# Kernel tuning notes

Measured on AMD Instinct MI355X. Metric: run time of the kernel, lower is better.

Reference implementation:

```python
import jax, jax.numpy as jnp
import numpy as np

N_NODES = 100000
N_EDGES = 1600000
IN_FEATS = 128
N_HIDDEN = 128
N_CLASSES = 47


def _glorot(key, shape):
    fan_in, fan_out = shape
    lim = jnp.sqrt(6.0 / (fan_in + fan_out))
    return jax.random.uniform(key, shape, jnp.float32, -lim, lim)


def setup_inputs() -> dict:
    key = jax.random.key(0)
    ks = jax.random.split(key, 12)
    x = jax.random.normal(ks[0], (N_NODES, IN_FEATS), jnp.float32)
    src = jax.random.randint(ks[1], (N_EDGES,), 0, N_NODES, jnp.int32)
    dst = jax.random.randint(ks[2], (N_EDGES,), 0, N_NODES, jnp.int32)
    dims = [(IN_FEATS, N_HIDDEN), (N_HIDDEN, N_HIDDEN), (N_HIDDEN, N_CLASSES)]
    params = {}
    for l, (di, do) in enumerate(dims):
        params[f"Ws{l}"] = _glorot(ks[3 + 3 * l], (di, do))
        params[f"Wn{l}"] = _glorot(ks[4 + 3 * l], (di, do))
        params[f"b{l}"] = jnp.zeros((do,), jnp.float32)
    return {"x": x, "src": src, "dst": dst, **params}


def _sage_layer(h, src, dst, Ws, Wn, b):
    # mean aggregation over incoming edges (irregular gather + segment-reduce)
    n = h.shape[0]
    msg = h[src]  # [E, F]
    agg = jax.ops.segment_sum(msg, dst, num_segments=n)
    deg = jax.ops.segment_sum(jnp.ones((src.shape[0],), h.dtype), dst, num_segments=n)
    agg = agg / jnp.maximum(deg, 1.0)[:, None]
    return h @ Ws + agg @ Wn + b


def reference(x, src, dst, Ws0, Wn0, b0, Ws1, Wn1, b1, Ws2, Wn2, b2):
    layers = [(Ws0, Wn0, b0), (Ws1, Wn1, b1), (Ws2, Wn2, b2)]
    h = x
    for l, (Ws, Wn, b) in enumerate(layers):
        h = _sage_layer(h, src, dst, Ws, Wn, b)
        if l != len(layers) - 1:
            h = jax.nn.relu(h)  # dropout is identity at inference
    return h
```

## Files before the change

kernel.cpp:

```cpp
#include <hip/hip_runtime.h>
#include <cstdint>
#include <cstddef>

static const int NN = 100000;
static const int NE = 1600000;
static const int F  = 128;
static const int BKT_SHIFT = 7;
static const int BNODES = 1 << BKT_SHIFT;
static const int NBKT = (NN + BNODES - 1) >> BKT_SHIFT;
static const int PKCAP = 4096;
static const int SRC_BITS = 17;
static const unsigned SRC_MASK = (1u << SRC_BITS) - 1u;

static const int GM = (NN + 127)/128;
static const int PREPW_B = 320;

typedef __attribute__((ext_vector_type(8))) short short8;
typedef __attribute__((ext_vector_type(4))) float float4v;
typedef __attribute__((ext_vector_type(2))) float f32x2;

static __device__ __forceinline__ unsigned f2bf(float f){
    unsigned u = __builtin_bit_cast(unsigned, f);
    return (u + 0x7FFFu + ((u >> 16) & 1u)) >> 16;
}
static __device__ __forceinline__ float bf_lo(unsigned u){
    return __builtin_bit_cast(float, u << 16);
}
static __device__ __forceinline__ float bf_hi(unsigned u){
    return __builtin_bit_cast(float, u & 0xFFFF0000u);
}


__global__ __launch_bounds__(256) void prep_fused_k(
        const int* __restrict__ src, const int* __restrict__ dst,
        int* __restrict__ bfill, unsigned* __restrict__ pk,
        const float* __restrict__ Ws0, const float* __restrict__ Wn0,
        const float* __restrict__ Ws1, const float* __restrict__ Wn1,
        const float* __restrict__ Ws2, const float* __restrict__ Wn2,
        unsigned short* __restrict__ Wt0, unsigned short* __restrict__ Wt1,
        unsigned short* __restrict__ Wt2){
    __shared__ int sh[2*NBKT];
    const int bid = blockIdx.x;
    const int t = threadIdx.x;
    if (bid < NBKT){
        int* hist  = sh;
        int* gbase = sh + NBKT;
        for (int i = t; i < NBKT; i += 256) hist[i] = 0;
        __syncthreads();
        const int e0 = bid * 2048;
        int s[8], d[8], b[8], r[8];
        #pragma unroll
        for (int j = 0; j < 8; ++j){
            int e = e0 + j*256 + t;
            if (e < NE){
                s[j] = src[e]; d[j] = dst[e];
                b[j] = d[j] >> BKT_SHIFT;
                r[j] = atomicAdd(&hist[b[j]], 1);
            }
        }
        __syncthreads();
        for (int i = t; i < NBKT; i += 256){
            int h = hist[i];
            int base = 0;
            if (h) base = atomicAdd(&bfill[i], h);
            gbase[i] = i*PKCAP + base;
        }
        __syncthreads();
        #pragma unroll
        for (int j = 0; j < 8; ++j){
            int e = e0 + j*256 + t;
            if (e < NE)
                pk[gbase[b[j]] + r[j]] =
                    (unsigned)s[j] | ((unsigned)(d[j] & (BNODES-1)) << SRC_BITS);
        }
    } else {
        int i = (bid - NBKT)*256 + t;
        const float* Ws; const float* Wn; unsigned short* Wt; int D; int idx;
        if (i < 32768){       Ws=Ws0; Wn=Wn0; Wt=Wt0; D=128; idx=i; }
        else if (i < 65536){  Ws=Ws1; Wn=Wn1; Wt=Wt1; D=128; idx=i-32768; }
        else {                Ws=Ws2; Wn=Wn2; Wt=Wt2; D=47;  idx=i-65536; }
        int n = idx >> 7, k = idx & 127;
        float v = 0.f;
        if (n < D)        v = Ws[k*D + n];
        else if (n < 2*D) v = Wn[k*D + (n - D)];
        Wt[n*128 + k] = (unsigned short)f2bf(v);
    }
}


template<int WN>
static __device__ __forceinline__ void gemm_core(char* ldsA,
        const unsigned short* __restrict__ Wt, const float* __restrict__ bias,
        unsigned short* __restrict__ Y, unsigned short* __restrict__ Z,
        int M, int D, int Dpad, int tile, int cbase){
    const int t = threadIdx.x;
    const int lane = t & 63;
    const int w = t >> 6;
    const int wm = w / WN, wn = w % WN;

    short8 bfrag[4][4];
    {
        int ncol = cbase + wn*64;
        #pragma unroll
        for (int n = 0; n < 4; ++n){
            int wrow = ncol + n*16 + (lane & 15);
            const unsigned short* bp = Wt + (size_t)wrow*128 + ((lane >> 4) * 8);
            #pragma unroll
            for (int kk = 0; kk < 4; ++kk)
                bfrag[n][kk] = *(const short8*)(bp + kk*32);
        }
    }

    float4v acc[4][4];
    #pragma unroll
    for (int m = 0; m < 4; ++m)
        #pragma unroll
        for (int n = 0; n < 4; ++n)
            acc[m][n] = (float4v){0.f,0.f,0.f,0.f};

    __syncthreads();

    #pragma unroll
    for (int m = 0; m < 4; ++m){
        int r = wm*64 + m*16 + (lane & 15);
        #pragma unroll
        for (int kk = 0; kk < 4; ++kk){
            int c = kk*4 + (lane >> 4);
            short8 a = *(const short8*)(ldsA + (size_t)r*256 + ((size_t)(c ^ (r & 7)) << 4));
            #pragma unroll
            for (int n = 0; n < 4; ++n)
                acc[m][n] = __builtin_amdgcn_mfma_f32_16x16x32_bf16(a, bfrag[n][kk], acc[m][n], 0, 0, 0);
        }
    }

    #pragma unroll
    for (int m = 0; m < 4; ++m){
        #pragma unroll
        for (int n = 0; n < 4; ++n){
            int c = cbase + wn*64 + n*16 + (lane & 15);
            #pragma unroll
            for (int j = 0; j < 4; ++j){
                int r = tile + wm*64 + m*16 + (lane >> 4)*4 + j;
                if (r < M){
                    float v = acc[m][n][j];
                    if (c < D){
                        v += bias[c];
                        Y[(size_t)r*Dpad + c] = (unsigned short)f2bf(v);
                    } else if (c < 2*D){
                        Z[(size_t)r*Dpad + (c - D)] = (unsigned short)f2bf(v);
                    }
                }
            }
        }
    }
}

template<int WAVES, int WN>
static __device__ __forceinline__ void gemm_body(char* ldsA,
        const unsigned short* __restrict__ hb, const unsigned short* __restrict__ Wt,
        const float* __restrict__ bias,
        unsigned short* __restrict__ Y, unsigned short* __restrict__ Z,
        int M, int D, int Dpad, int tile, int cbase){
    const int t = threadIdx.x;
    const int lane = t & 63;
    const int w = t >> 6;
    #pragma unroll
    for (int i = 0; i < 32/WAVES; ++i){
        int chunkid = i*WAVES + w;
        int lin = chunkid*64 + lane;
        int row = lin >> 4;
        int cs  = lin & 15;
        int grow = tile + row; if (grow >= M) grow = M - 1;
        const char* src = (const char*)hb + (size_t)grow*256 + ((size_t)(cs ^ (row & 7)) << 4);
        __builtin_amdgcn_global_load_lds(
            (const __attribute__((address_space(1))) void*)src,
            (__attribute__((address_space(3))) void*)(ldsA + (size_t)chunkid*1024 + (size_t)lane*16),
            16, 0, 0);
    }
    gemm_core<WN>(ldsA, Wt, bias, Y, Z, M, D, Dpad, tile, cbase);
}


__global__ __launch_bounds__(512) void sort_gemm_k(
        const unsigned* __restrict__ pk, const int* __restrict__ bfill,
        int* __restrict__ row_ptr, int* __restrict__ ssorted,
        const float* __restrict__ x, const unsigned short* __restrict__ Wt,
        const float* __restrict__ bias,
        unsigned short* __restrict__ Y, unsigned short* __restrict__ Z, int N){
    __shared__ char smem[128*256];
    const int bid = blockIdx.x;
    const int t = threadIdx.x;
    if (bid < NBKT){
        int* hc  = (int*)smem;
        int* of  = hc + 128;
        int* fi  = of + 128;
        int* red = fi + 128;
        const int b = bid;
        int part = 0;
        for (int i = t; i < b; i += 512) part += bfill[i];
        red[t] = part;
        if (t < 128){ hc[t] = 0; fi[t] = 0; }
        __syncthreads();
        for (int off = 256; off > 0; off >>= 1){
            if (t < off) red[t] += red[t+off];
            __syncthreads();
        }
        const int rbeg = red[0];
        const int cntb = bfill[b];
        const unsigned* mypk = pk + (size_t)b * PKCAP;
        for (int i = t; i < cntb; i += 512)
            atomicAdd(&hc[mypk[i] >> SRC_BITS], 1);
        __syncthreads();
        if (t < 128) of[t] = hc[t];
        __syncthreads();
        for (int off = 1; off < 128; off <<= 1){
            int add = (t < 128 && t >= off) ? of[t-off] : 0;
            __syncthreads();
            if (t < 128) of[t] += add;
            __syncthreads();
        }
        if (t < 128){
            int excl = of[t] - hc[t];
            of[t] = excl;
            int node = (b << BKT_SHIFT) + t;
            if (node < N) row_ptr[node] = rbeg + excl;
        }
        if (b == 0 && t == 0) row_ptr[N] = NE;
        __syncthreads();
        for (int i = t; i < cntb; i += 512){
            unsigned p = mypk[i];
            int dl = (int)(p >> SRC_BITS);
            int pos = rbeg + of[dl] + atomicAdd(&fi[dl], 1);
            ssorted[pos] = (int)(p & SRC_MASK);
        }
    } else {
        const int tile = (bid - NBKT) * 128;
        #pragma unroll
        for (int it = 0; it < 4; ++it){
            int lin = it*512 + t;
            int row = lin >> 4;
            int cs  = lin & 15;
            int grow = tile + row; if (grow >= N) grow = N - 1;
            int csg = cs ^ (row & 7);
            const float4* sp = (const float4*)((const char*)x + (size_t)grow*512 + (size_t)csg*32);
            float4 v0 = sp[0], v1 = sp[1];
            uint4 o;
            o.x = f2bf(v0.x) | (f2bf(v0.y) << 16);
            o.y = f2bf(v0.z) | (f2bf(v0.w) << 16);
            o.z = f2bf(v1.x) | (f2bf(v1.y) << 16);
            o.w = f2bf(v1.z) | (f2bf(v1.w) << 16);
            *(uint4*)(smem + (size_t)lin*16) = o;
        }
        gemm_core<4>(smem, Wt, bias, Y, Z, N, 128, 128, tile, 0);
    }
}

__global__ __launch_bounds__(512) void gemm512_k(
        const unsigned short* __restrict__ hb, const unsigned short* __restrict__ Wt,
        const float* __restrict__ bias,
        unsigned short* __restrict__ Y, unsigned short* __restrict__ Z,
        int M, int D, int Dpad){
    __shared__ char ldsA[128*256];
    gemm_body<8,4>(ldsA, hb, Wt, bias, Y, Z, M, D, Dpad, blockIdx.x*128, 0);
}

__global__ __launch_bounds__(256) void gemm256_k(
        const unsigned short* __restrict__ hb, const unsigned short* __restrict__ Wt,
        const float* __restrict__ bias,
        unsigned short* __restrict__ Y, unsigned short* __restrict__ Z,
        int M, int D, int Dpad){
    __shared__ char ldsA[128*256];
    gemm_body<4,2>(ldsA, hb, Wt, bias, Y, Z, M, D, Dpad, blockIdx.x*128, 0);
}


__global__ __launch_bounds__(256) void agg128_k(
        const unsigned short* __restrict__ Yb, const unsigned short* __restrict__ Zb,
        const int* __restrict__ row_ptr, const int* __restrict__ ssorted,
        unsigned short* __restrict__ hout, int N){
    const int lane = threadIdx.x & 63;
    const int q   = lane >> 4;
    const int sub = lane & 15;
    const int node = blockIdx.x*4 + (threadIdx.x >> 6);
    if (node >= N) return;
    const int beg = __builtin_amdgcn_readfirstlane(row_ptr[node]);
    const int end = __builtin_amdgcn_readfirstlane(row_ptr[node+1]);
    const float inv = 1.0f / fmaxf((float)(end - beg), 1.0f);
    const char* zc = (const char*)Zb;
    const unsigned boff = (unsigned)(sub*16);
    f32x2 a0={0.f,0.f}, a1={0.f,0.f}, a2={0.f,0.f}, a3={0.f,0.f};
    for (int e = beg; e < end; e += 32){
        int s[8];
        #pragma unroll
        for (int j = 0; j < 8; ++j){
            int ei = e + 4*j + q;
            int ec = ei < end ? ei : end - 1;
            s[j] = ssorted[ec];
        }
        uint4 u[8];
        #pragma unroll
        for (int j = 0; j < 8; ++j)
            u[j] = *(const uint4*)(zc + ((unsigned)s[j]*256u + boff));
        #pragma unroll
        for (int j = 0; j < 8; ++j){
            if (e + 4*j + q < end){
                a0 += (f32x2){ bf_lo(u[j].x), bf_hi(u[j].x) };
                a1 += (f32x2){ bf_lo(u[j].y), bf_hi(u[j].y) };
                a2 += (f32x2){ bf_lo(u[j].z), bf_hi(u[j].z) };
                a3 += (f32x2){ bf_lo(u[j].w), bf_hi(u[j].w) };
            }
        }
    }
    a0.x += __shfl_xor(a0.x,16,64); a0.x += __shfl_xor(a0.x,32,64);
    a0.y += __shfl_xor(a0.y,16,64); a0.y += __shfl_xor(a0.y,32,64);
    a1.x += __shfl_xor(a1.x,16,64); a1.x += __shfl_xor(a1.x,32,64);
    a1.y += __shfl_xor(a1.y,16,64); a1.y += __shfl_xor(a1.y,32,64);
    a2.x += __shfl_xor(a2.x,16,64); a2.x += __shfl_xor(a2.x,32,64);
    a2.y += __shfl_xor(a2.y,16,64); a2.y += __shfl_xor(a2.y,32,64);
    a3.x += __shfl_xor(a3.x,16,64); a3.x += __shfl_xor(a3.x,32,64);
    a3.y += __shfl_xor(a3.y,16,64); a3.y += __shfl_xor(a3.y,32,64);
    if (q == 0){
        uint4 yu = *(const uint4*)((const char*)Yb + (size_t)node*256 + sub*16);
        float r0 = fmaxf(bf_lo(yu.x) + a0.x*inv, 0.f);
        float r1 = fmaxf(bf_hi(yu.x) + a0.y*inv, 0.f);
        float r2 = fmaxf(bf_lo(yu.y) + a1.x*inv, 0.f);
        float r3 = fmaxf(bf_hi(yu.y) + a1.y*inv, 0.f);
        float r4 = fmaxf(bf_lo(yu.z) + a2.x*inv, 0.f);
        float r5 = fmaxf(bf_hi(yu.z) + a2.y*inv, 0.f);
        float r6 = fmaxf(bf_lo(yu.w) + a3.x*inv, 0.f);
        float r7 = fmaxf(bf_hi(yu.w) + a3.y*inv, 0.f);
        uint4 o;
        o.x = f2bf(r0) | (f2bf(r1) << 16);
        o.y = f2bf(r2) | (f2bf(r3) << 16);
        o.z = f2bf(r4) | (f2bf(r5) << 16);
        o.w = f2bf(r6) | (f2bf(r7) << 16);
        *(uint4*)((char*)hout + (size_t)node*256 + sub*16) = o;
    }
}

__global__ __launch_bounds__(256) void aggfin_k(
        const unsigned short* __restrict__ Yb, const unsigned short* __restrict__ Zb,
        const int* __restrict__ row_ptr, const int* __restrict__ ssorted,
        float* __restrict__ out, int N){
    const int lane = threadIdx.x & 63;
    const int slot = lane >> 3;
    const int sub  = lane & 7;
    const int node = blockIdx.x*4 + (threadIdx.x >> 6);
    if (node >= N) return;
    const int beg = __builtin_amdgcn_readfirstlane(row_ptr[node]);
    const int end = __builtin_amdgcn_readfirstlane(row_ptr[node+1]);
    const float inv = 1.0f / fmaxf((float)(end - beg), 1.0f);
    const char* zc = (const char*)Zb;
    const unsigned boff = (unsigned)(sub*16);
    f32x2 a0={0.f,0.f}, a1={0.f,0.f}, a2={0.f,0.f}, a3={0.f,0.f};
    for (int e = beg; e < end; e += 32){
        int s[4];
        #pragma unroll
        for (int j = 0; j < 4; ++j){
            int ei = e + 8*j + slot;
            int ec = ei < end ? ei : end - 1;
            s[j] = ssorted[ec];
        }
        uint4 u[4];
        #pragma unroll
        for (int j = 0; j < 4; ++j)
            u[j] = *(const uint4*)(zc + ((unsigned)s[j]*128u + boff));
        #pragma unroll
        for (int j = 0; j < 4; ++j){
            if (e + 8*j + slot < end){
                a0 += (f32x2){ bf_lo(u[j].x), bf_hi(u[j].x) };
                a1 += (f32x2){ bf_lo(u[j].y), bf_hi(u[j].y) };
                a2 += (f32x2){ bf_lo(u[j].z), bf_hi(u[j].z) };
                a3 += (f32x2){ bf_lo(u[j].w), bf_hi(u[j].w) };
            }
        }
    }
    a0.x += __shfl_xor(a0.x,8,64); a0.x += __shfl_xor(a0.x,16,64); a0.x += __shfl_xor(a0.x,32,64);
    a0.y += __shfl_xor(a0.y,8,64); a0.y += __shfl_xor(a0.y,16,64); a0.y += __shfl_xor(a0.y,32,64);
    a1.x += __shfl_xor(a1.x,8,64); a1.x += __shfl_xor(a1.x,16,64); a1.x += __shfl_xor(a1.x,32,64);
    a1.y += __shfl_xor(a1.y,8,64); a1.y += __shfl_xor(a1.y,16,64); a1.y += __shfl_xor(a1.y,32,64);
    a2.x += __shfl_xor(a2.x,8,64); a2.x += __shfl_xor(a2.x,16,64); a2.x += __shfl_xor(a2.x,32,64);
    a2.y += __shfl_xor(a2.y,8,64); a2.y += __shfl_xor(a2.y,16,64); a2.y += __shfl_xor(a2.y,32,64);
    a3.x += __shfl_xor(a3.x,8,64); a3.x += __shfl_xor(a3.x,16,64); a3.x += __shfl_xor(a3.x,32,64);
    a3.y += __shfl_xor(a3.y,8,64); a3.y += __shfl_xor(a3.y,16,64); a3.y += __shfl_xor(a3.y,32,64);
    if (slot == 0){
        uint4 yu = *(const uint4*)((const char*)Yb + (size_t)node*128 + sub*16);
        float v[8];
        v[0] = bf_lo(yu.x) + a0.x*inv;
        v[1] = bf_hi(yu.x) + a0.y*inv;
        v[2] = bf_lo(yu.y) + a1.x*inv;
        v[3] = bf_hi(yu.y) + a1.y*inv;
        v[4] = bf_lo(yu.z) + a2.x*inv;
        v[5] = bf_hi(yu.z) + a2.y*inv;
        v[6] = bf_lo(yu.w) + a3.x*inv;
        v[7] = bf_hi(yu.w) + a3.y*inv;
        int f = sub*8;
        size_t o = (size_t)node*47 + f;
        #pragma unroll
        for (int k = 0; k < 8; ++k)
            if (f + k < 47) out[o + k] = v[k];
    }
}


extern "C" void kernel_launch(void* const* d_in, const int* in_sizes, int n_in,
                              void* d_out, int out_size, void* d_ws, size_t ws_size,
                              hipStream_t stream){
    const float* x   = (const float*)d_in[0];
    const int*   src = (const int*)  d_in[1];
    const int*   dstv= (const int*)  d_in[2];
    const float* Ws0 = (const float*)d_in[3];
    const float* Wn0 = (const float*)d_in[4];
    const float* b0  = (const float*)d_in[5];
    const float* Ws1 = (const float*)d_in[6];
    const float* Wn1 = (const float*)d_in[7];
    const float* b1  = (const float*)d_in[8];
    const float* Ws2 = (const float*)d_in[9];
    const float* Wn2 = (const float*)d_in[10];
    const float* b2  = (const float*)d_in[11];
    float* out = (float*)d_out;
    const int N = NN;

    char* w = (char*)d_ws;
    size_t off = 0;
    auto alloc = [&](size_t bytes)->char*{
        char* p = w + off; off += (bytes + 255) & ~(size_t)255; return p;
    };
    int*   bfill   = (int*)  alloc((size_t)NBKT*4);
    int*   row_ptr = (int*)  alloc((size_t)(NN+1)*4);
    int*   ssorted = (int*)  alloc((size_t)NE*4);
    unsigned* pk   = (unsigned*)alloc((size_t)NBKT*PKCAP*4);
    unsigned short* hA  = (unsigned short*)alloc((size_t)NN*F*2);
    unsigned short* hB  = (unsigned short*)alloc((size_t)NN*F*2);
    unsigned short* Yb  = (unsigned short*)alloc((size_t)NN*F*2);
    unsigned short* Zb  = (unsigned short*)alloc((size_t)NN*F*2);
    unsigned short* Wt0 = (unsigned short*)alloc((size_t)256*128*2);
    unsigned short* Wt1 = (unsigned short*)alloc((size_t)256*128*2);
    unsigned short* Wt2 = (unsigned short*)alloc((size_t)128*128*2);
    (void)ws_size; (void)n_in; (void)in_sizes; (void)out_size;

    hipMemsetAsync(bfill, 0, (size_t)NBKT*4, stream);

    prep_fused_k<<<NBKT + PREPW_B, 256, 0, stream>>>(
        src, dstv, bfill, pk,
        Ws0, Wn0, Ws1, Wn1, Ws2, Wn2, Wt0, Wt1, Wt2);

    sort_gemm_k<<<NBKT + GM, 512, 0, stream>>>(
        pk, bfill, row_ptr, ssorted, x, Wt0, b0, Yb, Zb, N);

    const int GA = (N + 3)/4;

    agg128_k <<<GA, 256, 0, stream>>>(Yb, Zb, row_ptr, ssorted, hA, N);
    gemm512_k<<<GM, 512, 0, stream>>>(hA, Wt1, b1, Yb, Zb, N, 128, 128);
    agg128_k <<<GA, 256, 0, stream>>>(Yb, Zb, row_ptr, ssorted, hB, N);
    gemm256_k<<<GM, 256, 0, stream>>>(hB, Wt2, b2, Yb, Zb, N, 47, 64);
    aggfin_k <<<GA, 256, 0, stream>>>(Yb, Zb, row_ptr, ssorted, out, N);
}
```

Baseline: 338.0 us.

## Split aggregation feature halves across XCD groups for L2 locality

The 128-wide aggregation kernel now launches twice as many blocks. Each block handles one 64-feature half of a node's row, and the block index is decoded so that XCDs 0-3 take the first half and XCDs 4-7 the second. Each XCD's L2 therefore sees only half of the gathered Z rows, and a wave processes 8 edges per step with 8 lanes per edge. This is meant to raise L2 hit rates on the random neighbor gathers. The cost is duplicated row_ptr and index loads per node, an extra shuffle-reduction stage, and reliance on round-robin block-to-XCD dispatch.

```diff
diff --git a/kernel.cpp b/kernel.cpp
--- a/kernel.cpp
+++ b/kernel.cpp
@@ -279,21 +279,25 @@
         const int* __restrict__ row_ptr, const int* __restrict__ ssorted,
         unsigned short* __restrict__ hout, int N){
     const int lane = threadIdx.x & 63;
-    const int q   = lane >> 4;
-    const int sub = lane & 15;
-    const int node = blockIdx.x*4 + (threadIdx.x >> 6);
+    const int slot = lane >> 3;
+    const int sub  = lane & 7;
+    const int bid  = blockIdx.x;
+    const int xcd  = bid & 7;
+    const int half = xcd >> 2;
+    const int ng   = (bid >> 3)*4 + (xcd & 3);
+    const int node = ng*4 + (threadIdx.x >> 6);
     if (node >= N) return;
     const int beg = __builtin_amdgcn_readfirstlane(row_ptr[node]);
     const int end = __builtin_amdgcn_readfirstlane(row_ptr[node+1]);
     const float inv = 1.0f / fmaxf((float)(end - beg), 1.0f);
     const char* zc = (const char*)Zb;
-    const unsigned boff = (unsigned)(sub*16);
+    const unsigned boff = (unsigned)(half*128 + sub*16);
     f32x2 a0={0.f,0.f}, a1={0.f,0.f}, a2={0.f,0.f}, a3={0.f,0.f};
-    for (int e = beg; e < end; e += 32){
+    for (int e = beg; e < end; e += 64){
         int s[8];
         #pragma unroll
         for (int j = 0; j < 8; ++j){
-            int ei = e + 4*j + q;
+            int ei = e + 8*j + slot;
             int ec = ei < end ? ei : end - 1;
             s[j] = ssorted[ec];
         }
@@ -303,7 +307,7 @@
             u[j] = *(const uint4*)(zc + ((unsigned)s[j]*256u + boff));
         #pragma unroll
         for (int j = 0; j < 8; ++j){
-            if (e + 4*j + q < end){
+            if (e + 8*j + slot < end){
                 a0 += (f32x2){ bf_lo(u[j].x), bf_hi(u[j].x) };
                 a1 += (f32x2){ bf_lo(u[j].y), bf_hi(u[j].y) };
                 a2 += (f32x2){ bf_lo(u[j].z), bf_hi(u[j].z) };
@@ -311,16 +315,16 @@
             }
         }
     }
-    a0.x += __shfl_xor(a0.x,16,64); a0.x += __shfl_xor(a0.x,32,64);
-    a0.y += __shfl_xor(a0.y,16,64); a0.y += __shfl_xor(a0.y,32,64);
-    a1.x += __shfl_xor(a1.x,16,64); a1.x += __shfl_xor(a1.x,32,64);
-    a1.y += __shfl_xor(a1.y,16,64); a1.y += __shfl_xor(a1.y,32,64);
-    a2.x += __shfl_xor(a2.x,16,64); a2.x += __shfl_xor(a2.x,32,64);
-    a2.y += __shfl_xor(a2.y,16,64); a2.y += __shfl_xor(a2.y,32,64);
-    a3.x += __shfl_xor(a3.x,16,64); a3.x += __shfl_xor(a3.x,32,64);
-    a3.y += __shfl_xor(a3.y,16,64); a3.y += __shfl_xor(a3.y,32,64);
-    if (q == 0){
-        uint4 yu = *(const uint4*)((const char*)Yb + (size_t)node*256 + sub*16);
+    a0.x += __shfl_xor(a0.x,8,64); a0.x += __shfl_xor(a0.x,16,64); a0.x += __shfl_xor(a0.x,32,64);
+    a0.y += __shfl_xor(a0.y,8,64); a0.y += __shfl_xor(a0.y,16,64); a0.y += __shfl_xor(a0.y,32,64);
+    a1.x += __shfl_xor(a1.x,8,64); a1.x += __shfl_xor(a1.x,16,64); a1.x += __shfl_xor(a1.x,32,64);
+    a1.y += __shfl_xor(a1.y,8,64); a1.y += __shfl_xor(a1.y,16,64); a1.y += __shfl_xor(a1.y,32,64);
+    a2.x += __shfl_xor(a2.x,8,64); a2.x += __shfl_xor(a2.x,16,64); a2.x += __shfl_xor(a2.x,32,64);
+    a2.y += __shfl_xor(a2.y,8,64); a2.y += __shfl_xor(a2.y,16,64); a2.y += __shfl_xor(a2.y,32,64);
+    a3.x += __shfl_xor(a3.x,8,64); a3.x += __shfl_xor(a3.x,16,64); a3.x += __shfl_xor(a3.x,32,64);
+    a3.y += __shfl_xor(a3.y,8,64); a3.y += __shfl_xor(a3.y,16,64); a3.y += __shfl_xor(a3.y,32,64);
+    if (slot == 0){
+        uint4 yu = *(const uint4*)((const char*)Yb + (size_t)node*256 + boff);
         float r0 = fmaxf(bf_lo(yu.x) + a0.x*inv, 0.f);
         float r1 = fmaxf(bf_hi(yu.x) + a0.y*inv, 0.f);
         float r2 = fmaxf(bf_lo(yu.y) + a1.x*inv, 0.f);
@@ -334,7 +338,7 @@
         o.y = f2bf(r2) | (f2bf(r3) << 16);
         o.z = f2bf(r4) | (f2bf(r5) << 16);
         o.w = f2bf(r6) | (f2bf(r7) << 16);
-        *(uint4*)((char*)hout + (size_t)node*256 + sub*16) = o;
+        *(uint4*)((char*)hout + (size_t)node*256 + boff) = o;
     }
 }
 
@@ -448,11 +452,12 @@
     sort_gemm_k<<<NBKT + GM, 512, 0, stream>>>(
         pk, bfill, row_ptr, ssorted, x, Wt0, b0, Yb, Zb, N);
 
-    const int GA = (N + 3)/4;
-
-    agg128_k <<<GA, 256, 0, stream>>>(Yb, Zb, row_ptr, ssorted, hA, N);
+    const int GA  = (N + 3)/4;
+    const int GA2 = GA*2;
+
+    agg128_k <<<GA2, 256, 0, stream>>>(Yb, Zb, row_ptr, ssorted, hA, N);
     gemm512_k<<<GM, 512, 0, stream>>>(hA, Wt1, b1, Yb, Zb, N, 128, 128);
-    agg128_k <<<GA, 256, 0, stream>>>(Yb, Zb, row_ptr, ssorted, hB, N);
+    agg128_k <<<GA2, 256, 0, stream>>>(Yb, Zb, row_ptr, ssorted, hB, N);
     gemm256_k<<<GM, 256, 0, stream>>>(hB, Wt2, b2, Yb, Zb, N, 47, 64);
     aggfin_k <<<GA, 256, 0, stream>>>(Yb, Zb, row_ptr, ssorted, out, N);
 }
```

After: 398.5 us. 17.9% more time.
